# Optimization experiments

Measured on AMD Instinct MI355X. Metric: run time of the kernel, lower is better.

Reference implementation:

```python
import jax, jax.numpy as jnp
import numpy as np

IN_FEATURES = 4096
PADDED_DIM = 4096
K_HALF = PADDED_DIM // 2 + 1  # 2049
K = K_HALF
ALPHA_INIT = 1.0
INIT_SCALE = 0.1
BIAS_SCALE = 0.1
BATCH = 8192


def setup_inputs() -> dict:
    key = jax.random.key(0)
    kx, kr, ki, kb = jax.random.split(key, 4)
    x = jax.random.normal(kx, (BATCH, IN_FEATURES), dtype=jnp.float32)
    # Params initialized as in the module's __init__ (frequency-decayed scale)
    k_idx = jnp.arange(K_HALF, dtype=jnp.float32)
    prior_s = 1.0 / jnp.sqrt(1.0 + k_idx ** ALPHA_INIT)
    w_real = jax.random.normal(kr, (K_HALF,), dtype=jnp.float32) * (INIT_SCALE * prior_s)
    w_imag = jax.random.normal(ki, (K_HALF,), dtype=jnp.float32) * (INIT_SCALE * prior_s)
    w_imag = w_imag.at[0].set(0.0)
    w_imag = w_imag.at[-1].set(0.0)  # Nyquist bin (padded_dim even)
    bias = jax.random.normal(kb, (PADDED_DIM,), dtype=jnp.float32) * BIAS_SCALE
    return {"x": x, "w_real": w_real, "w_imag": w_imag, "bias": bias}


def _fourier_full(w_real, w_imag):
    # Mask frequencies >= K, then build full-length spectrum via Hermitian symmetry.
    mask = (jnp.arange(K_HALF) < K).astype(w_real.dtype)
    half = w_real * mask + 1j * (w_imag * mask)  # [k_half] complex
    nyq = half[-1].real[None].astype(half.dtype)  # real Nyquist bin
    full = jnp.concatenate([half[:-1], nyq, jnp.conj(half[1:-1])[::-1]])  # [padded_dim]
    return full


def reference(x, w_real, w_imag, bias):
    fft_full = _fourier_full(w_real, w_imag)  # [padded_dim] complex64
    # d_in == padded_dim -> no zero-padding needed (slice is a no-op, kept faithful)
    x_pad = x[..., :PADDED_DIM]
    Xf = jnp.fft.fft(x_pad, axis=-1)                 # [B, padded_dim] complex
    y = jnp.fft.ifft(Xf * fft_full[None, :], axis=-1).real  # [B, padded_dim]
    return y + bias[None, :]
```

## Files before the change

kernel.cpp:

```cpp
#include <hip/hip_runtime.h>
#include <math.h>

#define N 4096
#define THREADS 256
#define BATCH 8192

#define SWZ(i) ((i) ^ (((i) >> 4) & 15))
#define IDX16(p) ((((p) & 3) << 2) | ((p) >> 2))

__device__ __forceinline__ float2 cmul(float2 a, float2 b) {
    return make_float2(fmaf(a.x, b.x, -(a.y * b.y)), fmaf(a.x, b.y, a.y * b.x));
}

template<bool INV>
__device__ __forceinline__ void dft4(float2* v, int base, int stride) {
    float2 a = v[base], b = v[base + stride], c = v[base + 2 * stride], d = v[base + 3 * stride];
    float2 t0 = make_float2(a.x + c.x, a.y + c.y);
    float2 t1 = make_float2(a.x - c.x, a.y - c.y);
    float2 t2 = make_float2(b.x + d.x, b.y + d.y);
    float2 t3 = make_float2(b.x - d.x, b.y - d.y);
    float2 j3 = INV ? make_float2(-t3.y, t3.x) : make_float2(t3.y, -t3.x);
    v[base]              = make_float2(t0.x + t2.x, t0.y + t2.y);
    v[base + stride]     = make_float2(t1.x + j3.x, t1.y + j3.y);
    v[base + 2 * stride] = make_float2(t0.x - t2.x, t0.y - t2.y);
    v[base + 3 * stride] = make_float2(t1.x - j3.x, t1.y - j3.y);
}

template<bool INV>
__device__ __forceinline__ void tw16(float2* v) {
    const float C1 = 0.9238795325112867f;
    const float S1 = 0.3826834323650898f;
    const float R2 = 0.7071067811865476f;
    const float s = INV ? 1.0f : -1.0f;
    const float2 W1 = make_float2(C1, s * S1);
    const float2 W2 = make_float2(R2, s * R2);
    const float2 W3 = make_float2(S1, s * C1);
    const float2 W6 = make_float2(-R2, s * R2);
    const float2 W9 = make_float2(-C1, -s * S1);
    v[5]  = cmul(v[5],  W1);
    v[9]  = cmul(v[9],  W2);
    v[13] = cmul(v[13], W3);
    v[6]  = cmul(v[6],  W2);
    { float2 z = v[10]; v[10] = INV ? make_float2(-z.y, z.x) : make_float2(z.y, -z.x); }
    v[14] = cmul(v[14], W6);
    v[7]  = cmul(v[7],  W3);
    v[11] = cmul(v[11], W6);
    v[15] = cmul(v[15], W9);
}

template<bool INV>
__device__ __forceinline__ void dft16(float2* v) {
    #pragma unroll
    for (int n1 = 0; n1 < 4; ++n1) dft4<INV>(v, n1, 4);
    tw16<INV>(v);
    #pragma unroll
    for (int k2 = 0; k2 < 4; ++k2) dft4<INV>(v, 4 * k2, 1);
}

template<bool INV>
__device__ __forceinline__ void dft16_perm(float2* v) {
    #pragma unroll
    for (int n1 = 0; n1 < 4; ++n1) dft4<INV>(v, 4 * n1, 1);
    tw16<INV>(v);
    #pragma unroll
    for (int k2 = 0; k2 < 4; ++k2) dft4<INV>(v, k2, 4);
}

__global__ void prep_kernel(const float* __restrict__ wr, const float* __restrict__ wi,
                            float2* __restrict__ H, float2* __restrict__ tw) {
    int i = blockIdx.x * blockDim.x + threadIdx.x;
    if (i < N) {
        double ang = -2.0 * M_PI * (double)i / (double)N;
        tw[i] = make_float2((float)cos(ang), (float)sin(ang));
        float re, im;
        if (i <= N / 2) {
            re = wr[i];
            im = (i == N / 2) ? 0.0f : wi[i];
        } else {
            re = wr[N - i];
            im = -wi[N - i];
        }
        H[i] = make_float2(re, im);
    }
}

__global__ __launch_bounds__(THREADS, 4) void fft_conv_kernel(
        const float* __restrict__ x, const float2* __restrict__ H,
        const float2* __restrict__ tw, const float* __restrict__ bias,
        float* __restrict__ out) {
    __shared__ float2 lds[N];
    const int t = threadIdx.x;
    const long base1 = (long)(2 * blockIdx.x) * N;
    const long base2 = base1 + N;

    float2 v[16];

    #pragma unroll
    for (int r = 0; r < 16; ++r) {
        v[r].x = x[base1 + t + 256 * r];
        v[r].y = x[base2 + t + 256 * r];
    }

    dft16<false>(v);
    #pragma unroll
    for (int p = 1; p < 16; ++p)
        v[IDX16(p)] = cmul(v[IDX16(p)], tw[t * p]);
    #pragma unroll
    for (int p = 0; p < 16; ++p)
        lds[SWZ(16 * t + p)] = v[IDX16(p)];
    __syncthreads();

    #pragma unroll
    for (int r = 0; r < 16; ++r) v[r] = lds[SWZ(t + 256 * r)];
    __syncthreads();
    dft16<false>(v);
    {
        const int k = t & 15, j = t >> 4;
        #pragma unroll
        for (int p = 1; p < 16; ++p)
            v[IDX16(p)] = cmul(v[IDX16(p)], tw[16 * j * p]);
        #pragma unroll
        for (int p = 0; p < 16; ++p)
            lds[SWZ(k + 256 * j + 16 * p)] = v[IDX16(p)];
    }
    __syncthreads();

    #pragma unroll
    for (int r = 0; r < 16; ++r) v[r] = lds[SWZ(t + 256 * r)];
    __syncthreads();
    dft16<false>(v);
    #pragma unroll
    for (int q = 0; q < 16; ++q)
        v[q] = cmul(v[q], H[t + 256 * IDX16(q)]);

    dft16_perm<true>(v);
    #pragma unroll
    for (int p = 1; p < 16; ++p) {
        float2 w = tw[t * p]; w.y = -w.y;
        v[p] = cmul(v[p], w);
    }
    #pragma unroll
    for (int p = 0; p < 16; ++p)
        lds[SWZ(16 * t + p)] = v[p];
    __syncthreads();

    #pragma unroll
    for (int r = 0; r < 16; ++r) v[r] = lds[SWZ(t + 256 * r)];
    __syncthreads();
    dft16<true>(v);
    {
        const int k = t & 15, j = t >> 4;
        #pragma unroll
        for (int p = 1; p < 16; ++p) {
            float2 w = tw[16 * j * p]; w.y = -w.y;
            v[IDX16(p)] = cmul(v[IDX16(p)], w);
        }
        #pragma unroll
        for (int p = 0; p < 16; ++p)
            lds[SWZ(k + 256 * j + 16 * p)] = v[IDX16(p)];
    }
    __syncthreads();

    #pragma unroll
    for (int r = 0; r < 16; ++r) v[r] = lds[SWZ(t + 256 * r)];
    dft16<true>(v);
    const float inv = 1.0f / (float)N;
    #pragma unroll
    for (int p = 0; p < 16; ++p) {
        float2 val = v[IDX16(p)];
        float bb = bias[t + 256 * p];
        out[base1 + t + 256 * p] = fmaf(val.x, inv, bb);
        out[base2 + t + 256 * p] = fmaf(val.y, inv, bb);
    }
}

extern "C" void kernel_launch(void* const* d_in, const int* in_sizes, int n_in,
                              void* d_out, int out_size, void* d_ws, size_t ws_size,
                              hipStream_t stream) {
    const float* x  = (const float*)d_in[0];
    const float* wr = (const float*)d_in[1];
    const float* wi = (const float*)d_in[2];
    const float* bs = (const float*)d_in[3];
    float* out = (float*)d_out;

    float2* H  = (float2*)d_ws;
    float2* tw = (float2*)((char*)d_ws + (size_t)N * sizeof(float2));

    prep_kernel<<<dim3(N / THREADS), dim3(THREADS), 0, stream>>>(wr, wi, H, tw);
    fft_conv_kernel<<<dim3(BATCH / 2), dim3(THREADS), 0, stream>>>(x, H, tw, bs, out);
}
```

Baseline: 315.4 us.

## Restructure FFT exchanges: fewer barriers, recurrence twiddles, three-level LDS swizzle

Rewrites the LDS transpose pattern of the three-pass radix-16 FFT so each thread writes and reads indices that need only one barrier per exchange, removing the extra second __syncthreads after every read. Twiddles are now generated by complex-multiply recurrence from one loaded base twiddle per pass, replacing up to 15 global/cache twiddle loads per pass. The inverse passes apply conjugated twiddles before the DFT (decimation-in-frequency order). The swizzle gains a third XOR term to avoid bank conflicts on the new strides. Recurrence twiddles add small accumulated rounding error.

```diff
diff --git a/kernel.cpp b/kernel.cpp
--- a/kernel.cpp
+++ b/kernel.cpp
@@ -5,11 +5,14 @@
 #define THREADS 256
 #define BATCH 8192
 
-#define SWZ(i) ((i) ^ (((i) >> 4) & 15))
+#define SWZ(i) ((i) ^ (((i) >> 4) & 15) ^ (((i) >> 8) & 15))
 #define IDX16(p) ((((p) & 3) << 2) | ((p) >> 2))
 
 __device__ __forceinline__ float2 cmul(float2 a, float2 b) {
     return make_float2(fmaf(a.x, b.x, -(a.y * b.y)), fmaf(a.x, b.y, a.y * b.x));
+}
+__device__ __forceinline__ float2 cmulc(float2 a, float2 b) {
+    return make_float2(fmaf(a.x, b.x, a.y * b.y), fmaf(a.y, b.x, -(a.x * b.y)));
 }
 
 template<bool INV>
@@ -66,6 +69,28 @@
     for (int k2 = 0; k2 < 4; ++k2) dft4<INV>(v, k2, 4);
 }
 
+__device__ __forceinline__ void twiddle_fwd(float2* v, float2 w1) {
+    float2 w2 = cmul(w1, w1);
+    float2 wo = w1, we = w2;
+    v[IDX16(1)] = cmul(v[IDX16(1)], wo);
+    v[IDX16(2)] = cmul(v[IDX16(2)], we);
+    #pragma unroll
+    for (int p = 3; p < 16; p += 2) { wo = cmul(wo, w2); v[IDX16(p)] = cmul(v[IDX16(p)], wo); }
+    #pragma unroll
+    for (int p = 4; p < 16; p += 2) { we = cmul(we, w2); v[IDX16(p)] = cmul(v[IDX16(p)], we); }
+}
+
+__device__ __forceinline__ void twiddle_inv(float2* v, float2 w1) {
+    float2 w2 = cmul(w1, w1);
+    float2 wo = w1, we = w2;
+    v[1] = cmulc(v[1], wo);
+    v[2] = cmulc(v[2], we);
+    #pragma unroll
+    for (int p = 3; p < 16; p += 2) { wo = cmul(wo, w2); v[p] = cmulc(v[p], wo); }
+    #pragma unroll
+    for (int p = 4; p < 16; p += 2) { we = cmul(we, w2); v[p] = cmulc(v[p], we); }
+}
+
 __global__ void prep_kernel(const float* __restrict__ wr, const float* __restrict__ wi,
                             float2* __restrict__ H, float2* __restrict__ tw) {
     int i = blockIdx.x * blockDim.x + threadIdx.x;
@@ -89,9 +114,14 @@
         const float2* __restrict__ tw, const float* __restrict__ bias,
         float* __restrict__ out) {
     __shared__ float2 lds[N];
-    const int t = threadIdx.x;
+    const int t  = threadIdx.x;
+    const int i1 = t & 15;
+    const int hi = t >> 4;
     const long base1 = (long)(2 * blockIdx.x) * N;
     const long base2 = base1 + N;
+
+    const float2 w1 = tw[t];
+    const float2 wb = tw[16 * i1];
 
     float2 v[16];
 
@@ -102,75 +132,53 @@
     }
 
     dft16<false>(v);
-    #pragma unroll
-    for (int p = 1; p < 16; ++p)
-        v[IDX16(p)] = cmul(v[IDX16(p)], tw[t * p]);
+    twiddle_fwd(v, w1);
     #pragma unroll
     for (int p = 0; p < 16; ++p)
-        lds[SWZ(16 * t + p)] = v[IDX16(p)];
+        lds[SWZ(t + 256 * p)] = v[IDX16(p)];
     __syncthreads();
 
     #pragma unroll
-    for (int r = 0; r < 16; ++r) v[r] = lds[SWZ(t + 256 * r)];
-    __syncthreads();
+    for (int r = 0; r < 16; ++r) v[r] = lds[SWZ(i1 + 16 * r + 256 * hi)];
     dft16<false>(v);
-    {
-        const int k = t & 15, j = t >> 4;
-        #pragma unroll
-        for (int p = 1; p < 16; ++p)
-            v[IDX16(p)] = cmul(v[IDX16(p)], tw[16 * j * p]);
-        #pragma unroll
-        for (int p = 0; p < 16; ++p)
-            lds[SWZ(k + 256 * j + 16 * p)] = v[IDX16(p)];
-    }
+    twiddle_fwd(v, wb);
+    #pragma unroll
+    for (int p = 0; p < 16; ++p)
+        lds[SWZ(i1 + 16 * p + 256 * hi)] = v[IDX16(p)];
     __syncthreads();
 
     #pragma unroll
-    for (int r = 0; r < 16; ++r) v[r] = lds[SWZ(t + 256 * r)];
-    __syncthreads();
+    for (int j = 0; j < 16; ++j) v[j] = lds[SWZ(j + 16 * hi + 256 * i1)];
     dft16<false>(v);
     #pragma unroll
     for (int q = 0; q < 16; ++q)
         v[q] = cmul(v[q], H[t + 256 * IDX16(q)]);
-
     dft16_perm<true>(v);
     #pragma unroll
-    for (int p = 1; p < 16; ++p) {
-        float2 w = tw[t * p]; w.y = -w.y;
-        v[p] = cmul(v[p], w);
-    }
-    #pragma unroll
-    for (int p = 0; p < 16; ++p)
-        lds[SWZ(16 * t + p)] = v[p];
+    for (int j = 0; j < 16; ++j)
+        lds[SWZ(j + 16 * hi + 256 * i1)] = v[j];
     __syncthreads();
 
     #pragma unroll
-    for (int r = 0; r < 16; ++r) v[r] = lds[SWZ(t + 256 * r)];
-    __syncthreads();
+    for (int p = 0; p < 16; ++p) v[p] = lds[SWZ(i1 + 16 * p + 256 * hi)];
+    twiddle_inv(v, wb);
     dft16<true>(v);
-    {
-        const int k = t & 15, j = t >> 4;
-        #pragma unroll
-        for (int p = 1; p < 16; ++p) {
-            float2 w = tw[16 * j * p]; w.y = -w.y;
-            v[IDX16(p)] = cmul(v[IDX16(p)], w);
-        }
-        #pragma unroll
-        for (int p = 0; p < 16; ++p)
-            lds[SWZ(k + 256 * j + 16 * p)] = v[IDX16(p)];
-    }
+    #pragma unroll
+    for (int r = 0; r < 16; ++r)
+        lds[SWZ(i1 + 16 * r + 256 * hi)] = v[IDX16(r)];
     __syncthreads();
 
     #pragma unroll
-    for (int r = 0; r < 16; ++r) v[r] = lds[SWZ(t + 256 * r)];
+    for (int p = 0; p < 16; ++p) v[p] = lds[SWZ(t + 256 * p)];
+    twiddle_inv(v, w1);
     dft16<true>(v);
     const float inv = 1.0f / (float)N;
     #pragma unroll
-    for (int p = 0; p < 16; ++p) {
-        float2 val = v[IDX16(p)];
-        float bb = bias[t + 256 * p];
-        out[base1 + t + 256 * p] = fmaf(val.x, inv, bb);
-        out[base2 + t + 256 * p] = fmaf(val.y, inv, bb);
+    for (int r = 0; r < 16; ++r) {
+        float2 val = v[IDX16(r)];
+        float bb = bias[t + 256 * r];
+        out[base1 + t + 256 * r] = fmaf(val.x, inv, bb);
+        out[base2 + t + 256 * r] = fmaf(val.y, inv, bb);
     }
 }
 
```

Measured after the change: 326.0 us. 3.3% more time.
